# Optimization experiments

Measured on AMD Instinct MI355X. Metric: run time of the kernel, lower is better.

Reference implementation:

```python
import jax, jax.numpy as jnp
import numpy as np

B, W, L = 32768, 5, 20            # batch, words per example, max chars per word
WV, CV = 50000, 100               # word vocab, char vocab
CE, OC, K = 32, 30, 3             # char embed dim, conv out channels (=window_size), kernel
WE, HID, TAGS = 50, 100, 36       # word embed dim, fc1 hidden, output tags


def setup_inputs() -> dict:
    key = jax.random.key(0)
    ks = jax.random.split(key, 8)
    inp = jax.random.randint(ks[0], (B, W, 1 + L), 0, 100, dtype=jnp.int32)
    embedding_matrix = jax.random.normal(ks[1], (WV, WE), jnp.float32).at[0].set(0.0)  # padding_idx=0, frozen
    char_emb = jax.random.normal(ks[2], (CV, CE), jnp.float32).at[0].set(0.0)          # padding_idx=0
    conv_w = jax.random.normal(ks[3], (OC, CE, K), jnp.float32) * 0.1
    conv_b = jnp.zeros((OC,), jnp.float32)
    fc1_w = jax.random.normal(ks[4], (HID, (WE + OC) * W), jnp.float32) * 0.05
    fc1_b = jnp.zeros((HID,), jnp.float32)
    out_w = jax.random.normal(ks[5], (TAGS, HID), jnp.float32) * 0.1
    out_b = jnp.zeros((TAGS,), jnp.float32)
    return dict(input=inp, embedding_matrix=embedding_matrix, char_emb=char_emb,
                conv_w=conv_w, conv_b=conv_b, fc1_w=fc1_w, fc1_b=fc1_b,
                out_w=out_w, out_b=out_b)


def reference(input, embedding_matrix, char_emb, conv_w, conv_b, fc1_w, fc1_b, out_w, out_b):
    b = input.shape[0]
    word_ids = input[:, :, 0]                 # [B, W]
    char_ids = input[:, :, 1:]                # [B, W, L]
    we = embedding_matrix[word_ids]           # [B, W, 50]
    ce = char_emb[char_ids]                   # [B, W, L, CE]
    # conv1d over char axis, batched over all B*W words at once
    x = ce.reshape(b * W, L, CE).transpose(0, 2, 1)        # [B*W, CE, L]
    conv = jax.lax.conv_general_dilated(
        x, conv_w, window_strides=(1,), padding='VALID',
        dimension_numbers=('NCH', 'OIH', 'NCH')) + conv_b[None, :, None]  # [B*W, OC, L-2]
    pooled = conv.max(axis=2).reshape(b, W, OC)            # max pool over time
    feats = jnp.concatenate([we, pooled], axis=-1).reshape(b, -1)  # [B, (50+OC)*W]
    h = jnp.tanh(feats @ fc1_w.T + fc1_b)     # dropout is a no-op at inference
    return h @ out_w.T + out_b                # [B, 36]
```

## Files before the change

### kernel.cpp

```cpp
#include <hip/hip_runtime.h>
#include <hip/hip_bf16.h>

#define B_TOT 32768
#define W 5
#define OC 30
#define WE 50
#define HID 100
#define TAGS 36

#define NI 32
#define FS 212
#define HS 68

#define WS_FC1_DW 9600
#define WS_OUT_DW 32896

typedef __attribute__((ext_vector_type(8))) short short8;
typedef __attribute__((ext_vector_type(4))) float f32x4;

__device__ inline unsigned short f2bf(float f) {
    __hip_bfloat16 h = __float2bfloat16(f);
    return *reinterpret_cast<unsigned short*>(&h);
}
__device__ inline unsigned int pk_bf16(float a, float b) {
    return (unsigned int)f2bf(a) | ((unsigned int)f2bf(b) << 16);
}
__device__ inline short8 as8(uint4 u) {
    union { uint4 a; short8 b; } v; v.a = u; return v.b;
}

__global__ void prep(const float* __restrict__ conv_w,
                     const float* __restrict__ char_emb,
                     const float* __restrict__ fc1_w,
                     const float* __restrict__ out_w,
                     unsigned int* __restrict__ ws) {
    int idx = blockIdx.x * 256 + threadIdx.x;
    if (idx < 9600) {
        int oc = idx & 31, c = (idx >> 5) % 100, k = idx / 3200;
        float s = 0.f;
        if (oc < OC) {
            for (int ce = 0; ce < 32; ++ce)
                s += char_emb[c * 32 + ce] * conv_w[(oc * 32 + ce) * 3 + k];
        }
        ((float*)ws)[idx] = s;
    } else if (idx < 9600 + 23296) {
        int t = idx - 9600;
        int dw = t & 3, lane = (t >> 2) & 63, chunk = t >> 8;
        int ks = chunk % 13, nt = chunk / 13;
        int j = nt * 16 + (lane & 15);
        int k = ks * 32 + (lane >> 4) * 8 + dw * 2;
        float a = (j < HID && k     < 400) ? fc1_w[j * 400 + k]     : 0.f;
        float b = (j < HID && k + 1 < 400) ? fc1_w[j * 400 + k + 1] : 0.f;
        ws[WS_FC1_DW + t] = pk_bf16(a, b);
    } else if (idx < 9600 + 23296 + 3072) {
        int t = idx - (9600 + 23296);
        int dw = t & 3, lane = (t >> 2) & 63, chunk = t >> 8;
        int ks = chunk % 4, nt = chunk / 4;
        int j = nt * 16 + (lane & 15);
        int k = ks * 32 + (lane >> 4) * 8 + dw * 2;
        float a = (j < TAGS && k     < HID) ? out_w[j * 100 + k]     : 0.f;
        float b = (j < TAGS && k + 1 < HID) ? out_w[j * 100 + k + 1] : 0.f;
        ws[WS_OUT_DW + t] = pk_bf16(a, b);
    }
}

__global__ __launch_bounds__(256)
void pos_fused(const int*   __restrict__ input,
               const float* __restrict__ emb,
               const float* __restrict__ conv_b,
               const float* __restrict__ fc1_b,
               const float* __restrict__ out_b,
               const unsigned int* __restrict__ ws,
               float*       __restrict__ out)
{
    __shared__ unsigned int F[NI * FS];
    __shared__ float        Tsf[9600];
    __shared__ unsigned int Hh[NI * HS];

    const int tid   = threadIdx.x;
    const int item0 = blockIdx.x * NI;

    for (int idx = tid; idx < 9600; idx += 256) Tsf[idx] = ((const float*)ws)[idx];
    for (int idx = tid; idx < NI * 12; idx += 256) F[(idx / 12) * FS + 200 + idx % 12] = 0;
    for (int idx = tid; idx < NI * 18; idx += 256) Hh[(idx / 18) * HS + 50 + idx % 18] = 0;

    for (int idx = tid; idx < NI * 5 * 25; idx += 256) {
        int ph = idx % 25;
        int w  = (idx / 25) % 5;
        int i  = idx / 125;
        int wid = input[(item0 + i) * 105 + w * 21];
        float2 e = *(const float2*)&emb[wid * 50 + ph * 2];
        F[i * FS + w * 40 + ph] = pk_bf16(e.x, e.y);
    }
    __syncthreads();

    {
        const int q8  = tid & 7;
        const int grp = tid >> 3;
        const int oc0 = q8 * 4;
        for (int round = 0; round < 5; ++round) {
            int task = round * 32 + grp;
            int i = task / 5, w = task % 5;
            const int* cp = &input[(item0 + i) * 105 + w * 21 + 1];
            int c[20];
            #pragma unroll
            for (int p = 0; p < 20; ++p) c[p] = cp[p];
            float m0 = -1e30f, m1 = -1e30f, m2 = -1e30f, m3 = -1e30f;
            #pragma unroll
            for (int p = 0; p < 18; ++p) {
                float4 t0 = *(const float4*)&Tsf[(       c[p    ]) * 32 + oc0];
                float4 t1 = *(const float4*)&Tsf[(3200 + c[p + 1] * 32) + oc0];
                float4 t2 = *(const float4*)&Tsf[(6400 + c[p + 2] * 32) + oc0];
                float s0 = t0.x + t1.x + t2.x;
                float s1 = t0.y + t1.y + t2.y;
                float s2 = t0.z + t1.z + t2.z;
                float s3 = t0.w + t1.w + t2.w;
                m0 = fmaxf(m0, s0); m1 = fmaxf(m1, s1);
                m2 = fmaxf(m2, s2); m3 = fmaxf(m3, s3);
            }
            float b0 = conv_b[oc0], b1 = conv_b[oc0 + 1];
            F[i * FS + w * 40 + 25 + q8 * 2] = pk_bf16(m0 + b0, m1 + b1);
            if (oc0 + 2 < OC) {
                float b2 = conv_b[oc0 + 2], b3 = conv_b[oc0 + 3];
                F[i * FS + w * 40 + 25 + q8 * 2 + 1] = pk_bf16(m2 + b2, m3 + b3);
            }
        }
    }
    __syncthreads();

    const int wv   = tid >> 6;
    const int lane = tid & 63;
    const int ln15 = lane & 15;
    const int quad = lane >> 4;
    {
        const int msub = wv & 1;
        const int nh   = wv >> 1;
        const int nt0  = nh * 4;
        const int NT   = nh ? 3 : 4;
        const int m0   = msub * 16;
        f32x4 acc[4] = {f32x4{0,0,0,0}, f32x4{0,0,0,0}, f32x4{0,0,0,0}, f32x4{0,0,0,0}};
        const uint4* wp = (const uint4*)(ws + WS_FC1_DW);
        const int aoff = (m0 + ln15) * FS + quad * 4;
        for (int ks = 0; ks < 13; ++ks) {
            short8 a = as8(*(const uint4*)&F[aoff + ks * 16]);
            #pragma unroll
            for (int t = 0; t < 4; ++t) {
                if (t < NT) {
                    uint4 bv = wp[((nt0 + t) * 13 + ks) * 64 + lane];
                    acc[t] = __builtin_amdgcn_mfma_f32_16x16x32_bf16(a, as8(bv), acc[t], 0, 0, 0);
                }
            }
        }
        #pragma unroll
        for (int t = 0; t < 4; ++t) {
            if (t < NT) {
                int j = (nt0 + t) * 16 + ln15;
                if (j < HID) {
                    float bj = fc1_b[j];
                    #pragma unroll
                    for (int r = 0; r < 4; ++r) {
                        int it = m0 + quad * 4 + r;
                        float hv = tanhf(acc[t][r] + bj);
                        ((unsigned short*)Hh)[it * (HS * 2) + j] = f2bf(hv);
                    }
                }
            }
        }
    }
    __syncthreads();

    {
        const int msub = wv & 1;
        const int nh   = wv >> 1;
        const int nt0  = nh * 2;
        const int NT   = nh ? 1 : 2;
        const int m0   = msub * 16;
        f32x4 acc[2] = {f32x4{0,0,0,0}, f32x4{0,0,0,0}};
        const uint4* wp = (const uint4*)(ws + WS_OUT_DW);
        const int aoff = (m0 + ln15) * HS + quad * 4;
        #pragma unroll
        for (int ks = 0; ks < 4; ++ks) {
            short8 a = as8(*(const uint4*)&Hh[aoff + ks * 16]);
            #pragma unroll
            for (int t = 0; t < 2; ++t) {
                if (t < NT) {
                    uint4 bv = wp[((nt0 + t) * 4 + ks) * 64 + lane];
                    acc[t] = __builtin_amdgcn_mfma_f32_16x16x32_bf16(a, as8(bv), acc[t], 0, 0, 0);
                }
            }
        }
        #pragma unroll
        for (int t = 0; t < 2; ++t) {
            if (t < NT) {
                int o = (nt0 + t) * 16 + ln15;
                if (o < TAGS) {
                    float bo = out_b[o];
                    #pragma unroll
                    for (int r = 0; r < 4; ++r) {
                        int it = item0 + m0 + quad * 4 + r;
                        out[it * TAGS + o] = acc[t][r] + bo;
                    }
                }
            }
        }
    }
}

extern "C" void kernel_launch(void* const* d_in, const int* in_sizes, int n_in,
                              void* d_out, int out_size, void* d_ws, size_t ws_size,
                              hipStream_t stream) {
    const int*   input  = (const int*)  d_in[0];
    const float* emb    = (const float*)d_in[1];
    const float* char_e = (const float*)d_in[2];
    const float* conv_w = (const float*)d_in[3];
    const float* conv_b = (const float*)d_in[4];
    const float* fc1_w  = (const float*)d_in[5];
    const float* fc1_b  = (const float*)d_in[6];
    const float* out_w  = (const float*)d_in[7];
    const float* out_b  = (const float*)d_in[8];
    unsigned int* ws = (unsigned int*)d_ws;

    prep<<<141, 256, 0, stream>>>(conv_w, char_e, fc1_w, out_w, ws);
    pos_fused<<<B_TOT / NI, 256, 0, stream>>>(input, emb, conv_b, fc1_b, out_b,
                                              ws, (float*)d_out);
}
```

Before: 133.7 us.

## Precompute pairwise char-tap sums table to cut conv lookups per position

Splits the weight preprocessing into two kernels and builds a 100x100x32 table of summed tap-0 and tap-1 char projections in global memory, so each conv position needs one global float4 load plus one swizzled LDS load instead of three LDS loads. The per-block LDS copy shrinks from the full 9600-float table to a rotated tap-2 table of 3200 floats, which allows a launch-bounds occupancy hint of 3 blocks per CU. The cost is a 1.28 MB table read through cache with random access and an extra prep kernel launch. Bias loads are hoisted out of the loop and the unroll of the position loop is reduced.

```diff
diff --git a/kernel.cpp b/kernel.cpp
--- a/kernel.cpp
+++ b/kernel.cpp
@@ -2,9 +2,7 @@
 #include <hip/hip_bf16.h>
 
 #define B_TOT 32768
-#define W 5
 #define OC 30
-#define WE 50
 #define HID 100
 #define TAGS 36
 
@@ -12,8 +10,11 @@
 #define FS 212
 #define HS 68
 
-#define WS_FC1_DW 9600
-#define WS_OUT_DW 32896
+#define WS_T01 0
+#define WS_T2R 320000
+#define WS_FC1 323200
+#define WS_OUT 346496
+#define WS_TK  349568
 
 typedef __attribute__((ext_vector_type(8))) short short8;
 typedef __attribute__((ext_vector_type(4))) float f32x4;
@@ -29,42 +30,58 @@
     union { uint4 a; short8 b; } v; v.a = u; return v.b;
 }
 
-__global__ void prep(const float* __restrict__ conv_w,
-                     const float* __restrict__ char_emb,
-                     const float* __restrict__ fc1_w,
-                     const float* __restrict__ out_w,
-                     unsigned int* __restrict__ ws) {
+__global__ void prep1(const float* __restrict__ conv_w,
+                      const float* __restrict__ char_emb,
+                      float* __restrict__ tk) {
     int idx = blockIdx.x * 256 + threadIdx.x;
-    if (idx < 9600) {
-        int oc = idx & 31, c = (idx >> 5) % 100, k = idx / 3200;
-        float s = 0.f;
-        if (oc < OC) {
-            for (int ce = 0; ce < 32; ++ce)
-                s += char_emb[c * 32 + ce] * conv_w[(oc * 32 + ce) * 3 + k];
-        }
-        ((float*)ws)[idx] = s;
-    } else if (idx < 9600 + 23296) {
-        int t = idx - 9600;
+    if (idx >= 9600) return;
+    int oc = idx & 31, c = (idx >> 5) % 100, k = idx / 3200;
+    float s = 0.f;
+    if (oc < OC) {
+        for (int ce = 0; ce < 32; ++ce)
+            s += char_emb[c * 32 + ce] * conv_w[(oc * 32 + ce) * 3 + k];
+    }
+    tk[idx] = s;
+}
+
+__global__ void prep2(const float* __restrict__ fc1_w,
+                      const float* __restrict__ out_w,
+                      unsigned int* __restrict__ ws) {
+    int idx = blockIdx.x * 256 + threadIdx.x;
+    const float* tk = (const float*)ws + WS_TK;
+    float* wsf = (float*)ws;
+    if (idx < 320000) {
+        int oc = idx & 31, pair = idx >> 5;
+        int c1 = pair % 100, c0 = pair / 100;
+        wsf[WS_T01 + idx] = tk[c0 * 32 + oc] + tk[3200 + c1 * 32 + oc];
+    } else if (idx < 323200) {
+        int t = idx - 320000;
+        int dw = t & 31, c = t >> 5;
+        int blk = dw >> 2, d = dw & 3;
+        int oc = (((blk - c) & 7) << 2) + d;
+        wsf[WS_T2R + t] = tk[6400 + c * 32 + oc];
+    } else if (idx < 323200 + 23296) {
+        int t = idx - 323200;
         int dw = t & 3, lane = (t >> 2) & 63, chunk = t >> 8;
         int ks = chunk % 13, nt = chunk / 13;
         int j = nt * 16 + (lane & 15);
         int k = ks * 32 + (lane >> 4) * 8 + dw * 2;
         float a = (j < HID && k     < 400) ? fc1_w[j * 400 + k]     : 0.f;
         float b = (j < HID && k + 1 < 400) ? fc1_w[j * 400 + k + 1] : 0.f;
-        ws[WS_FC1_DW + t] = pk_bf16(a, b);
-    } else if (idx < 9600 + 23296 + 3072) {
-        int t = idx - (9600 + 23296);
+        ws[WS_FC1 + t] = pk_bf16(a, b);
+    } else if (idx < 346496 + 3072) {
+        int t = idx - 346496;
         int dw = t & 3, lane = (t >> 2) & 63, chunk = t >> 8;
         int ks = chunk % 4, nt = chunk / 4;
         int j = nt * 16 + (lane & 15);
         int k = ks * 32 + (lane >> 4) * 8 + dw * 2;
         float a = (j < TAGS && k     < HID) ? out_w[j * 100 + k]     : 0.f;
         float b = (j < TAGS && k + 1 < HID) ? out_w[j * 100 + k + 1] : 0.f;
-        ws[WS_OUT_DW + t] = pk_bf16(a, b);
-    }
-}
-
-__global__ __launch_bounds__(256)
+        ws[WS_OUT + t] = pk_bf16(a, b);
+    }
+}
+
+__global__ __launch_bounds__(256, 3)
 void pos_fused(const int*   __restrict__ input,
                const float* __restrict__ emb,
                const float* __restrict__ conv_b,
@@ -74,13 +91,14 @@
                float*       __restrict__ out)
 {
     __shared__ unsigned int F[NI * FS];
-    __shared__ float        Tsf[9600];
+    __shared__ float        T2s[3200];
     __shared__ unsigned int Hh[NI * HS];
 
     const int tid   = threadIdx.x;
     const int item0 = blockIdx.x * NI;
-
-    for (int idx = tid; idx < 9600; idx += 256) Tsf[idx] = ((const float*)ws)[idx];
+    const float* wsf = (const float*)ws;
+
+    for (int idx = tid; idx < 3200; idx += 256) T2s[idx] = wsf[WS_T2R + idx];
     for (int idx = tid; idx < NI * 12; idx += 256) F[(idx / 12) * FS + 200 + idx % 12] = 0;
     for (int idx = tid; idx < NI * 18; idx += 256) Hh[(idx / 18) * HS + 50 + idx % 18] = 0;
 
@@ -98,6 +116,11 @@
         const int q8  = tid & 7;
         const int grp = tid >> 3;
         const int oc0 = q8 * 4;
+        const float4* t01 = (const float4*)(wsf + WS_T01);
+        const float b0 = conv_b[oc0];
+        const float b1 = conv_b[oc0 + 1];
+        const float b2 = (oc0 + 2 < OC) ? conv_b[oc0 + 2] : 0.f;
+        const float b3 = (oc0 + 3 < OC) ? conv_b[oc0 + 3] : 0.f;
         for (int round = 0; round < 5; ++round) {
             int task = round * 32 + grp;
             int i = task / 5, w = task % 5;
@@ -106,24 +129,19 @@
             #pragma unroll
             for (int p = 0; p < 20; ++p) c[p] = cp[p];
             float m0 = -1e30f, m1 = -1e30f, m2 = -1e30f, m3 = -1e30f;
-            #pragma unroll
+            #pragma unroll 6
             for (int p = 0; p < 18; ++p) {
-                float4 t0 = *(const float4*)&Tsf[(       c[p    ]) * 32 + oc0];
-                float4 t1 = *(const float4*)&Tsf[(3200 + c[p + 1] * 32) + oc0];
-                float4 t2 = *(const float4*)&Tsf[(6400 + c[p + 2] * 32) + oc0];
-                float s0 = t0.x + t1.x + t2.x;
-                float s1 = t0.y + t1.y + t2.y;
-                float s2 = t0.z + t1.z + t2.z;
-                float s3 = t0.w + t1.w + t2.w;
-                m0 = fmaxf(m0, s0); m1 = fmaxf(m1, s1);
-                m2 = fmaxf(m2, s2); m3 = fmaxf(m3, s3);
-            }
-            float b0 = conv_b[oc0], b1 = conv_b[oc0 + 1];
+                float4 a = t01[(c[p] * 100 + c[p + 1]) * 8 + q8];
+                int c2 = c[p + 2];
+                float4 b = *(const float4*)&T2s[c2 * 32 + (((q8 + c2) & 7) << 2)];
+                m0 = fmaxf(m0, a.x + b.x);
+                m1 = fmaxf(m1, a.y + b.y);
+                m2 = fmaxf(m2, a.z + b.z);
+                m3 = fmaxf(m3, a.w + b.w);
+            }
             F[i * FS + w * 40 + 25 + q8 * 2] = pk_bf16(m0 + b0, m1 + b1);
-            if (oc0 + 2 < OC) {
-                float b2 = conv_b[oc0 + 2], b3 = conv_b[oc0 + 3];
+            if (oc0 + 2 < OC)
                 F[i * FS + w * 40 + 25 + q8 * 2 + 1] = pk_bf16(m2 + b2, m3 + b3);
-            }
         }
     }
     __syncthreads();
@@ -139,7 +157,7 @@
         const int NT   = nh ? 3 : 4;
         const int m0   = msub * 16;
         f32x4 acc[4] = {f32x4{0,0,0,0}, f32x4{0,0,0,0}, f32x4{0,0,0,0}, f32x4{0,0,0,0}};
-        const uint4* wp = (const uint4*)(ws + WS_FC1_DW);
+        const uint4* wp = (const uint4*)(ws + WS_FC1);
         const int aoff = (m0 + ln15) * FS + quad * 4;
         for (int ks = 0; ks < 13; ++ks) {
             short8 a = as8(*(const uint4*)&F[aoff + ks * 16]);
@@ -176,7 +194,7 @@
         const int NT   = nh ? 1 : 2;
         const int m0   = msub * 16;
         f32x4 acc[2] = {f32x4{0,0,0,0}, f32x4{0,0,0,0}};
-        const uint4* wp = (const uint4*)(ws + WS_OUT_DW);
+        const uint4* wp = (const uint4*)(ws + WS_OUT);
         const int aoff = (m0 + ln15) * HS + quad * 4;
         #pragma unroll
         for (int ks = 0; ks < 4; ++ks) {
@@ -220,7 +238,8 @@
     const float* out_b  = (const float*)d_in[8];
     unsigned int* ws = (unsigned int*)d_ws;
 
-    prep<<<141, 256, 0, stream>>>(conv_w, char_e, fc1_w, out_w, ws);
+    prep1<<<38, 256, 0, stream>>>(conv_w, char_e, (float*)ws + WS_TK);
+    prep2<<<1366, 256, 0, stream>>>(fc1_w, out_w, ws);
     pos_fused<<<B_TOT / NI, 256, 0, stream>>>(input, emb, conv_b, fc1_b, out_b,
                                               ws, (float*)d_out);
 }
```

After: 140.2 us. 1.05x slower.
